# Performance work log

Measured on AMD Instinct MI355X. Metric: run time of the kernel, lower is better.

Reference implementation:

```python
import jax, jax.numpy as jnp
import numpy as np
from jax import lax

K = 10
EPS = 1e-12

def _l2norm(v):
    # F.normalize: v / max(||v||_2, eps) along last dim
    n = jnp.sqrt(jnp.sum(v * v, axis=-1, keepdims=True))
    return v / jnp.maximum(n, EPS)

def setup_inputs() -> dict:
    key = jax.random.key(0)
    ks = jax.random.split(key, 10)
    N, F_in, H, C, E = 100000, 512, 128, 40, 1600000
    x = jax.random.normal(ks[0], (N, F_in), dtype=jnp.float32)
    edge_index = jax.random.randint(ks[1], (2, E), 0, N, dtype=jnp.int64)
    s1 = 1.0 / np.sqrt(F_in)
    W1 = jax.random.uniform(ks[2], (F_in, H), jnp.float32, -s1, s1)
    b1 = jax.random.uniform(ks[3], (H,), jnp.float32, -s1, s1)
    s2 = 1.0 / np.sqrt(H)
    proj_w = jax.random.uniform(ks[4], (H, 1), jnp.float32, -s2, s2)
    proj_b = jax.random.uniform(ks[5], (1,), jnp.float32, -s2, s2)
    hop_w = jax.random.normal(ks[6], (1, K + 1), dtype=jnp.float32) * 0.1  # glorot-ish
    W2 = jax.random.uniform(ks[7], (H, C), jnp.float32, -s2, s2)
    b2 = jax.random.uniform(ks[8], (C,), jnp.float32, -s2, s2)
    return {"x": x, "edge_index": edge_index, "W1": W1, "b1": b1,
            "proj_w": proj_w, "proj_b": proj_b, "hop_w": hop_w,
            "W2": W2, "b2": b2}

def reference(x, edge_index, W1, b1, proj_w, proj_b, hop_w, W2, b2):
    N = x.shape[0]
    # Net: dropout (eval -> identity), lin1 + selu
    h = jax.nn.selu(x @ W1 + b1)  # [N, H]

    # --- gcn_norm with added self-loops ---
    loops = jnp.arange(N, dtype=edge_index.dtype)
    row = jnp.concatenate([edge_index[0], loops])
    col = jnp.concatenate([edge_index[1], loops])
    ew = jnp.ones(row.shape[0], dtype=h.dtype)
    deg = jax.ops.segment_sum(ew, col, num_segments=N)  # [N]
    dinv = jnp.where(deg > 0, lax.rsqrt(deg), 0.0)
    norm = dinv[row] * ew * dinv[col]  # [E+N]

    # --- K hops of scatter-add propagation ---
    def hop(xc, _):
        xn = jax.ops.segment_sum(norm[:, None] * xc[row], col, num_segments=N)
        return xn, xn
    _, hops = lax.scan(hop, h, None, length=K)  # [K, N, H]
    pps = jnp.concatenate([h[None], hops], axis=0).transpose(1, 0, 2)  # [N, K+1, H]

    # attention-weighted hop pooling
    feature_pool = (pps @ proj_w + proj_b)[..., 0]      # [N, K+1]
    m = feature_pool.mean(axis=0)                        # [K+1]
    share_w = _l2norm(m + hop_w)                         # [1, K+1]
    self_w = _l2norm(feature_pool)                       # [N, K+1]
    share = jnp.einsum('k,nkh->nh', share_w[0], pps)     # [N, H]
    selfr = jnp.einsum('nk,nkh->nh', self_w, pps)        # [N, H]
    out_prop = 0.2 * share + 0.8 * selfr

    h2 = jnp.tanh(out_prop)
    logits = h2 @ W2 + b2
    return jax.nn.log_softmax(logits, axis=1)
```

## Files before the change

kernel.cpp:

```cpp
#include <hip/hip_runtime.h>

typedef unsigned int uint;
typedef unsigned short ushort;

typedef short short8 __attribute__((ext_vector_type(8)));
typedef float floatx4 __attribute__((ext_vector_type(4)));

#define FIN 512
#define HF  128
#define NC  40
#define KHOPS 10

__device__ __forceinline__ ushort f2bf(float f) {
    uint u = __float_as_uint(f);
    uint r = (u + 0x7fffu + ((u >> 16) & 1u)) >> 16;
    return (ushort)r;
}
__device__ __forceinline__ float bflo(uint v) { return __uint_as_float(v << 16); }
__device__ __forceinline__ float bfhi(uint v) { return __uint_as_float(v & 0xffff0000u); }
__device__ __forceinline__ uint packbf2(float a, float b) {
    return (uint)f2bf(a) | ((uint)f2bf(b) << 16);
}
__device__ __forceinline__ float selu_f(float v) {
    const float l = 1.0507009873554805f, a = 1.6732632423543772f;
    return v > 0.f ? l * v : l * a * (expf(v) - 1.f);
}

__global__ void k_w1frag(const float* __restrict__ W1, ushort* __restrict__ w1f) {
    int id = blockIdx.x * 256 + threadIdx.x;
    if (id >= 16 * 8 * 64) return;
    int l = id & 63;
    int t = (id >> 6) & 7;
    int s = id >> 9;
    int row0 = s * 32 + (l >> 4) * 8;
    int col  = t * 16 + (l & 15);
    ushort* dst = w1f + (size_t)id * 8;
#pragma unroll
    for (int i = 0; i < 8; ++i)
        dst[i] = f2bf(W1[(row0 + i) * HF + col]);
}

__global__ void k_w2frag(const float* __restrict__ W2, ushort* __restrict__ w2f) {
    int id = blockIdx.x * 256 + threadIdx.x;
    if (id >= 12 * 64) return;
    int l = id & 63;
    int tile = id >> 6;
    int kk = tile / 3, t = tile % 3;
    int row0 = kk * 32 + (l >> 4) * 8;
    int col  = t * 16 + (l & 15);
    ushort* dst = w2f + (size_t)id * 8;
#pragma unroll
    for (int i = 0; i < 8; ++i)
        dst[i] = (col < NC) ? f2bf(W2[(row0 + i) * NC + col]) : (ushort)0;
}

__global__ void k_gemm(const float* __restrict__ x, const ushort* __restrict__ w1f,
                       const float* __restrict__ b1, ushort* __restrict__ h, int N) {
    __shared__ __align__(16) ushort As[64 * 64];
    int tid = threadIdx.x;
    int lane = tid & 63, w = tid >> 6;
    int rowblk = blockIdx.x * 64;

    floatx4 acc[8];
#pragma unroll
    for (int t = 0; t < 8; ++t) acc[t] = (floatx4){0.f, 0.f, 0.f, 0.f};

    for (int kk = 0; kk < 8; ++kk) {
#pragma unroll
        for (int i = 0; i < 4; ++i) {
            int li = tid + 256 * i;
            int r = li >> 4, c4 = li & 15;
            float4 v = make_float4(0.f, 0.f, 0.f, 0.f);
            if (rowblk + r < N)
                v = *(const float4*)(x + (size_t)(rowblk + r) * FIN + kk * 64 + c4 * 4);
            uint p0 = packbf2(v.x, v.y);
            uint p1 = packbf2(v.z, v.w);
            int byteoff = (r * 128 + c4 * 8) ^ ((r & 7) << 4);
            *(uint2*)((char*)As + byteoff) = make_uint2(p0, p1);
        }
        __syncthreads();
        int rowA = w * 16 + (lane & 15);
#pragma unroll
        for (int s = 0; s < 2; ++s) {
            int aoff = (rowA * 128 + s * 64 + (lane >> 4) * 16) ^ ((rowA & 7) << 4);
            short8 af = *(const short8*)((const char*)As + aoff);
#pragma unroll
            for (int t = 0; t < 8; ++t) {
                const short8 bf = *(const short8*)(w1f + ((size_t)((kk * 2 + s) * 8 + t) * 64 + lane) * 8);
                acc[t] = __builtin_amdgcn_mfma_f32_16x16x32_bf16(af, bf, acc[t], 0, 0, 0);
            }
        }
        __syncthreads();
    }
#pragma unroll
    for (int t = 0; t < 8; ++t) {
        int col = t * 16 + (lane & 15);
        float bias = b1[col];
#pragma unroll
        for (int q = 0; q < 4; ++q) {
            int row = rowblk + w * 16 + (lane >> 4) * 4 + q;
            if (row < N) {
                float v = selu_f(acc[t][q] + bias);
                h[(size_t)row * HF + col] = f2bf(v);
            }
        }
    }
}

__global__ void k_deg_init(int* __restrict__ deg, int N) {
    int i = blockIdx.x * 256 + threadIdx.x;
    if (i < N) deg[i] = 1;
}
__global__ void k_deg(const int* __restrict__ ei, int* __restrict__ deg, int E) {
    int e = blockIdx.x * 256 + threadIdx.x;
    if (e < E) atomicAdd(&deg[ei[E + e]], 1);
}
__global__ void k_dinv(const int* __restrict__ deg, float* __restrict__ dinv, int N) {
    int i = blockIdx.x * 256 + threadIdx.x;
    if (i < N) dinv[i] = rsqrtf((float)deg[i]);
}

__global__ void k_scan1(const int* __restrict__ deg, int* __restrict__ offs,
                        int* __restrict__ bsum, int N) {
    __shared__ int lds[256];
    int tid = threadIdx.x;
    int base = blockIdx.x * 1024;
    int c[4], s = 0;
#pragma unroll
    for (int i = 0; i < 4; ++i) {
        int g = base + tid * 4 + i;
        c[i] = (g < N) ? (deg[g] - 1) : 0;
        s += c[i];
    }
    lds[tid] = s;
    __syncthreads();
    for (int off = 1; off < 256; off <<= 1) {
        int add = (tid >= off) ? lds[tid - off] : 0;
        __syncthreads();
        lds[tid] += add;
        __syncthreads();
    }
    int run = lds[tid] - s;
#pragma unroll
    for (int i = 0; i < 4; ++i) {
        int g = base + tid * 4 + i;
        if (g < N) offs[g] = run;
        run += c[i];
    }
    if (tid == 0) bsum[blockIdx.x] = lds[255];
}
__global__ void k_scan2(int* __restrict__ bsum, int nb) {
    if (blockIdx.x == 0 && threadIdx.x == 0) {
        int run = 0;
        for (int i = 0; i < nb; ++i) { int v = bsum[i]; bsum[i] = run; run += v; }
    }
}
__global__ void k_scan3(int* __restrict__ offs, const int* __restrict__ bsum, int N, int E) {
    int g = blockIdx.x * 256 + threadIdx.x;
    if (g < N) offs[g] += bsum[g >> 10];
    else if (g == N) offs[N] = E;
}

__global__ void k_fill(const int* __restrict__ ei, const int* __restrict__ offs,
                       int* __restrict__ cursor, int2* __restrict__ edat,
                       const float* __restrict__ dinv, int E) {
    int e = blockIdx.x * 256 + threadIdx.x;
    if (e >= E) return;
    int r = ei[e], c = ei[E + e];
    int p = offs[c] + atomicAdd(&cursor[c], 1);
    edat[p] = make_int2(r, __float_as_int(dinv[r] * dinv[c]));
}

__global__ void k_fp0(const ushort* __restrict__ h, const float* __restrict__ projw,
                      const float* __restrict__ projb, float* __restrict__ fp0, int N) {
    int wid = (blockIdx.x * blockDim.x + threadIdx.x) >> 6;
    int lane = threadIdx.x & 63;
    if (wid >= N) return;
    uint v = ((const uint*)h)[(size_t)wid * 64 + lane];
    float dot = bflo(v) * projw[2 * lane] + bfhi(v) * projw[2 * lane + 1];
#pragma unroll
    for (int m = 1; m < 64; m <<= 1) dot += __shfl_xor(dot, m);
    if (lane == 0) fp0[wid] = dot + projb[0];
}

__global__ __launch_bounds__(256) void k_hop(
                      const ushort* __restrict__ xin, ushort* __restrict__ xout,
                      const int* __restrict__ offs, const int2* __restrict__ edat,
                      const float* __restrict__ dinv,
                      const float* __restrict__ projw, const float* __restrict__ projb,
                      float* __restrict__ fpk, int N) {
    int wid = (blockIdx.x * blockDim.x + threadIdx.x) >> 6;
    int lane = threadIdx.x & 63;
    if (wid >= N) return;
    const uint* xin2 = (const uint*)xin;
    float dn = dinv[wid];
    uint sv = xin2[(size_t)wid * 64 + lane];
    float wself = dn * dn;
    float acc0 = wself * bflo(sv);
    float acc1 = wself * bfhi(sv);
    int s = offs[wid], e = offs[wid + 1];
    for (int base = s; base < e; base += 64) {
        int idx = base + lane;
        int idxc = min(idx, e - 1);
        int2 ed = edat[idxc];
        int src = ed.x;
        float ew = (idx < e) ? __int_as_float(ed.y) : 0.f;
        int cnt = min(64, e - base);
        int groups = (cnt + 15) >> 4;
        for (int g = 0; g < groups; ++g) {
            int j = g * 16;
            uint xv[16];
            float wv[16];
#pragma unroll
            for (int u = 0; u < 16; ++u) {
                int sj = __builtin_amdgcn_readlane(src, j + u);
                wv[u] = __int_as_float(__builtin_amdgcn_readlane(__float_as_int(ew), j + u));
                xv[u] = xin2[(size_t)(uint)sj * 64 + lane];
            }
#pragma unroll
            for (int u = 0; u < 16; ++u) {
                acc0 = fmaf(wv[u], bflo(xv[u]), acc0);
                acc1 = fmaf(wv[u], bfhi(xv[u]), acc1);
            }
        }
    }
    ((uint*)xout)[(size_t)wid * 64 + lane] = packbf2(acc0, acc1);
    float dot = acc0 * projw[2 * lane] + acc1 * projw[2 * lane + 1];
#pragma unroll
    for (int m = 1; m < 64; m <<= 1) dot += __shfl_xor(dot, m);
    if (lane == 0) fpk[wid] = dot + projb[0];
}

__global__ void k_msum(const float* __restrict__ fp, float* __restrict__ msum, int N) {
    int k = blockIdx.y;
    int i = blockIdx.x * 256 + threadIdx.x;
    int tid = threadIdx.x;
    float v = (i < N) ? fp[(size_t)k * N + i] : 0.f;
#pragma unroll
    for (int m = 1; m < 64; m <<= 1) v += __shfl_xor(v, m);
    __shared__ float ws4[4];
    if ((tid & 63) == 0) ws4[tid >> 6] = v;
    __syncthreads();
    if (tid == 0) atomicAdd(&msum[k], ws4[0] + ws4[1] + ws4[2] + ws4[3]);
}

__global__ void k_sharew(const float* __restrict__ msum, const float* __restrict__ hopw,
                         float* __restrict__ sharew, int N) {
    int k = threadIdx.x;
    float s = (k < KHOPS + 1) ? (msum[k] / (float)N + hopw[k]) : 0.f;
    float ss = s * s;
#pragma unroll
    for (int m = 1; m < 64; m <<= 1) ss += __shfl_xor(ss, m);
    float inv = 1.f / fmaxf(sqrtf(ss), 1e-12f);
    if (k < KHOPS + 1) sharew[k] = s * inv;
}

__global__ __launch_bounds__(256) void k_out(
                     const ushort* __restrict__ hops, const float* __restrict__ fp,
                     const float* __restrict__ sharew, const ushort* __restrict__ w2f,
                     const float* __restrict__ b2, float* __restrict__ out, int N) {
    __shared__ __align__(16) char As[16 * 256];
    int tid = threadIdx.x;
    int nloc = tid >> 4;
    int fg = tid & 15;
    int node = blockIdx.x * 16 + nloc;
    bool valid = node < N;
    int nodec = valid ? node : N - 1;
    const uint* hops2 = (const uint*)hops;

    float c[KHOPS + 1];
    float ss = 0.f;
#pragma unroll
    for (int k = 0; k <= KHOPS; ++k) {
        float f = fp[(size_t)k * N + nodec];
        c[k] = f;
        ss += f * f;
    }
    float inv = 1.f / fmaxf(sqrtf(ss), 1e-12f);
#pragma unroll
    for (int k = 0; k <= KHOPS; ++k)
        c[k] = valid ? (0.2f * sharew[k] + 0.8f * c[k] * inv) : 0.f;

    const uint* base = hops2 + (size_t)nodec * 64 + fg * 4;
    size_t kstr = (size_t)N * 64;
    float a[8];
#pragma unroll
    for (int j = 0; j < 8; ++j) a[j] = 0.f;
#pragma unroll
    for (int k = 0; k <= KHOPS; ++k) {
        uint4 v = *(const uint4*)(base + (size_t)k * kstr);
        float ck = c[k];
        a[0] = fmaf(ck, bflo(v.x), a[0]);
        a[1] = fmaf(ck, bfhi(v.x), a[1]);
        a[2] = fmaf(ck, bflo(v.y), a[2]);
        a[3] = fmaf(ck, bfhi(v.y), a[3]);
        a[4] = fmaf(ck, bflo(v.z), a[4]);
        a[5] = fmaf(ck, bfhi(v.z), a[5]);
        a[6] = fmaf(ck, bflo(v.w), a[6]);
        a[7] = fmaf(ck, bfhi(v.w), a[7]);
    }
    uint4 pk;
    pk.x = packbf2(tanhf(a[0]), tanhf(a[1]));
    pk.y = packbf2(tanhf(a[2]), tanhf(a[3]));
    pk.z = packbf2(tanhf(a[4]), tanhf(a[5]));
    pk.w = packbf2(tanhf(a[6]), tanhf(a[7]));
    {
        int slotbyte = fg * 16;
        int addr = nloc * 256 + (slotbyte ^ ((nloc & 15) << 4));
        *(uint4*)(As + addr) = pk;
    }
    __syncthreads();

    int w = tid >> 6, lane = tid & 63;
    floatx4 acc = (floatx4){0.f, 0.f, 0.f, 0.f};
    if (w < 3) {
        int r = lane & 15;
#pragma unroll
        for (int kk = 0; kk < 4; ++kk) {
            int slotbyte = kk * 64 + (lane >> 4) * 16;
            int addr = r * 256 + (slotbyte ^ ((r & 15) << 4));
            short8 af = *(const short8*)(As + addr);
            const short8 bf = *(const short8*)(w2f + (size_t)((kk * 3 + w) * 64 + lane) * 8);
            acc = __builtin_amdgcn_mfma_f32_16x16x32_bf16(af, bf, acc, 0, 0, 0);
        }
    }
    __syncthreads();

    float* Ls = (float*)As;
    if (w < 3) {
        int cls = w * 16 + (lane & 15);
        float bb = (cls < NC) ? b2[cls] : 0.f;
#pragma unroll
        for (int q = 0; q < 4; ++q) {
            int row = (lane >> 4) * 4 + q;
            Ls[row * 48 + cls] = acc[q] + bb;
        }
    }
    __syncthreads();

    int r2 = tid >> 4;
    int c16 = tid & 15;
    float v0 = Ls[r2 * 48 + c16];
    float v1 = Ls[r2 * 48 + 16 + c16];
    bool has2 = c16 < 8;
    float v2 = has2 ? Ls[r2 * 48 + 32 + c16] : -INFINITY;
    float lm = fmaxf(fmaxf(v0, v1), v2);
#pragma unroll
    for (int m = 1; m < 16; m <<= 1) lm = fmaxf(lm, __shfl_xor(lm, m));
    float se = expf(v0 - lm) + expf(v1 - lm) + (has2 ? expf(v2 - lm) : 0.f);
#pragma unroll
    for (int m = 1; m < 16; m <<= 1) se += __shfl_xor(se, m);
    float lse = lm + logf(se);
    int nodeo = blockIdx.x * 16 + r2;
    if (nodeo < N) {
        out[(size_t)nodeo * NC + c16] = v0 - lse;
        out[(size_t)nodeo * NC + 16 + c16] = v1 - lse;
        if (has2) out[(size_t)nodeo * NC + 32 + c16] = v2 - lse;
    }
}

extern "C" void kernel_launch(void* const* d_in, const int* in_sizes, int n_in,
                              void* d_out, int out_size, void* d_ws, size_t ws_size,
                              hipStream_t stream) {
    const float* x     = (const float*)d_in[0];
    const int*   ei    = (const int*)d_in[1];
    const float* W1    = (const float*)d_in[2];
    const float* b1    = (const float*)d_in[3];
    const float* projw = (const float*)d_in[4];
    const float* projb = (const float*)d_in[5];
    const float* hopw  = (const float*)d_in[6];
    const float* W2    = (const float*)d_in[7];
    const float* b2    = (const float*)d_in[8];
    float* out = (float*)d_out;

    int N = in_sizes[0] / FIN;
    int E = in_sizes[1] / 2;

    char* p = (char*)d_ws;
    auto alloc = [&](size_t bytes) -> char* {
        char* r = p;
        p += (bytes + 255) & ~(size_t)255;
        return r;
    };
    ushort* hops   = (ushort*)alloc((size_t)(KHOPS + 1) * N * HF * 2);
    int*    deg    = (int*)alloc((size_t)N * 4);
    float*  dinv   = (float*)alloc((size_t)N * 4);
    int*    offs   = (int*)alloc((size_t)(N + 1) * 4);
    int*    cursor = (int*)alloc((size_t)N * 4);
    int*    bsum   = (int*)alloc(4096);
    int2*   edat   = (int2*)alloc((size_t)E * 8);
    float*  fp     = (float*)alloc((size_t)(KHOPS + 1) * N * 4);
    float*  msum   = (float*)alloc(64);
    float*  sharew = (float*)alloc(64);
    ushort* w1f    = (ushort*)alloc((size_t)FIN * HF * 2);
    ushort* w2f    = (ushort*)alloc((size_t)12 * 64 * 8 * 2);

    int nb256N = (N + 255) / 256;
    int nbE    = (E + 255) / 256;
    int nbWave = (N + 3) / 4;
    int nb1024 = (N + 1023) / 1024;

    k_w1frag<<<32, 256, 0, stream>>>(W1, w1f);
    k_w2frag<<<3, 256, 0, stream>>>(W2, w2f);
    k_gemm<<<(N + 63) / 64, 256, 0, stream>>>(x, w1f, b1, hops, N);

    k_deg_init<<<nb256N, 256, 0, stream>>>(deg, N);
    k_deg<<<nbE, 256, 0, stream>>>(ei, deg, E);
    k_dinv<<<nb256N, 256, 0, stream>>>(deg, dinv, N);

    k_scan1<<<nb1024, 256, 0, stream>>>(deg, offs, bsum, N);
    k_scan2<<<1, 64, 0, stream>>>(bsum, nb1024);
    k_scan3<<<(N + 256) / 256, 256, 0, stream>>>(offs, bsum, N, E);

    hipMemsetAsync(cursor, 0, (size_t)N * 4, stream);
    k_fill<<<nbE, 256, 0, stream>>>(ei, offs, cursor, edat, dinv, E);

    k_fp0<<<nbWave, 256, 0, stream>>>(hops, projw, projb, fp, N);

    for (int k = 1; k <= KHOPS; ++k) {
        const ushort* xin = hops + (size_t)(k - 1) * N * HF;
        ushort* xout      = hops + (size_t)k * N * HF;
        k_hop<<<nbWave, 256, 0, stream>>>(xin, xout, offs, edat, dinv,
                                          projw, projb, fp + (size_t)k * N, N);
    }

    hipMemsetAsync(msum, 0, 64, stream);
    dim3 gm(nb256N, KHOPS + 1);
    k_msum<<<gm, 256, 0, stream>>>(fp, msum, N);
    k_sharew<<<1, 64, 0, stream>>>(msum, hopw, sharew, N);

    k_out<<<(N + 15) / 16, 256, 0, stream>>>(hops, fp, sharew, w2f, b2, out, N);
}
```

Baseline: 1.009 ms.

## Rewrite lin1 GEMM without LDS, fuse fp0 projection, widen hop gather batches

The lin1 GEMM drops its shared-memory staging. Each wave now loads x rows straight into registers, converts them with v_cvt_pk_bf16_f32, and software-prefetches the next K slice of A and the W1 fragments. Each wave covers 32 rows, so a block covers 128. The hop-0 projection dot product is computed in the GEMM epilogue, which removes the separate k_fp0 kernel and its re-read of h. The hop kernel now handles small neighbor lists with one 16-wide batch and larger ones in 32-wide batches, putting more gathers in flight at the cost of more registers.

```diff
diff --git a/kernel.cpp b/kernel.cpp
--- a/kernel.cpp
+++ b/kernel.cpp
@@ -5,6 +5,7 @@
 
 typedef short short8 __attribute__((ext_vector_type(8)));
 typedef float floatx4 __attribute__((ext_vector_type(4)));
+typedef uint uintx4 __attribute__((ext_vector_type(4)));
 
 #define FIN 512
 #define HF  128
@@ -20,6 +21,11 @@
 __device__ __forceinline__ float bfhi(uint v) { return __uint_as_float(v & 0xffff0000u); }
 __device__ __forceinline__ uint packbf2(float a, float b) {
     return (uint)f2bf(a) | ((uint)f2bf(b) << 16);
+}
+__device__ __forceinline__ uint cvtpk(float lo, float hi) {
+    uint r;
+    asm("v_cvt_pk_bf16_f32 %0, %1, %2" : "=v"(r) : "v"(lo), "v"(hi));
+    return r;
 }
 __device__ __forceinline__ float selu_f(float v) {
     const float l = 1.0507009873554805f, a = 1.6732632423543772f;
@@ -54,56 +60,113 @@
         dst[i] = (col < NC) ? f2bf(W2[(row0 + i) * NC + col]) : (ushort)0;
 }
 
-__global__ void k_gemm(const float* __restrict__ x, const ushort* __restrict__ w1f,
-                       const float* __restrict__ b1, ushort* __restrict__ h, int N) {
-    __shared__ __align__(16) ushort As[64 * 64];
+__global__ __launch_bounds__(256) void k_gemm(
+        const float* __restrict__ x, const ushort* __restrict__ w1f,
+        const float* __restrict__ b1, ushort* __restrict__ h,
+        const float* __restrict__ projw, const float* __restrict__ projb,
+        float* __restrict__ fp0, int N) {
     int tid = threadIdx.x;
     int lane = tid & 63, w = tid >> 6;
-    int rowblk = blockIdx.x * 64;
-
-    floatx4 acc[8];
-#pragma unroll
-    for (int t = 0; t < 8; ++t) acc[t] = (floatx4){0.f, 0.f, 0.f, 0.f};
-
-    for (int kk = 0; kk < 8; ++kk) {
-#pragma unroll
-        for (int i = 0; i < 4; ++i) {
-            int li = tid + 256 * i;
-            int r = li >> 4, c4 = li & 15;
-            float4 v = make_float4(0.f, 0.f, 0.f, 0.f);
-            if (rowblk + r < N)
-                v = *(const float4*)(x + (size_t)(rowblk + r) * FIN + kk * 64 + c4 * 4);
-            uint p0 = packbf2(v.x, v.y);
-            uint p1 = packbf2(v.z, v.w);
-            int byteoff = (r * 128 + c4 * 8) ^ ((r & 7) << 4);
-            *(uint2*)((char*)As + byteoff) = make_uint2(p0, p1);
-        }
-        __syncthreads();
-        int rowA = w * 16 + (lane & 15);
-#pragma unroll
-        for (int s = 0; s < 2; ++s) {
-            int aoff = (rowA * 128 + s * 64 + (lane >> 4) * 16) ^ ((rowA & 7) << 4);
-            short8 af = *(const short8*)((const char*)As + aoff);
-#pragma unroll
-            for (int t = 0; t < 8; ++t) {
-                const short8 bf = *(const short8*)(w1f + ((size_t)((kk * 2 + s) * 8 + t) * 64 + lane) * 8);
-                acc[t] = __builtin_amdgcn_mfma_f32_16x16x32_bf16(af, bf, acc[t], 0, 0, 0);
+    int rowblk = blockIdx.x * 128 + w * 32;
+    int kq = (lane >> 4) * 8;
+
+    int r0 = rowblk + (lane & 15);
+    int r1 = r0 + 16;
+    size_t r0c = (size_t)min(r0, N - 1) * FIN;
+    size_t r1c = (size_t)min(r1, N - 1) * FIN;
+
+    floatx4 acc[2][8];
+#pragma unroll
+    for (int rt = 0; rt < 2; ++rt)
+#pragma unroll
+        for (int t = 0; t < 8; ++t) acc[rt][t] = (floatx4){0.f, 0.f, 0.f, 0.f};
+
+    float4 aC[4];
+    short8 bC[8];
+    {
+        const float* p0 = x + r0c + kq;
+        const float* p1 = x + r1c + kq;
+        aC[0] = *(const float4*)p0; aC[1] = *(const float4*)(p0 + 4);
+        aC[2] = *(const float4*)p1; aC[3] = *(const float4*)(p1 + 4);
+        const ushort* wp = w1f + ((size_t)lane) * 8;
+#pragma unroll
+        for (int t = 0; t < 8; ++t) bC[t] = *(const short8*)(wp + (size_t)t * 512);
+    }
+
+#pragma unroll 1
+    for (int kk = 0; kk < 16; ++kk) {
+        float4 aN[4];
+        short8 bN[8];
+        if (kk < 15) {
+            int kb = (kk + 1) * 32 + kq;
+            const float* p0 = x + r0c + kb;
+            const float* p1 = x + r1c + kb;
+            aN[0] = *(const float4*)p0; aN[1] = *(const float4*)(p0 + 4);
+            aN[2] = *(const float4*)p1; aN[3] = *(const float4*)(p1 + 4);
+            const ushort* wp = w1f + ((size_t)((kk + 1) * 8) * 64 + lane) * 8;
+#pragma unroll
+            for (int t = 0; t < 8; ++t) bN[t] = *(const short8*)(wp + (size_t)t * 512);
+        }
+        uintx4 pa0, pa1;
+        pa0.x = cvtpk(aC[0].x, aC[0].y); pa0.y = cvtpk(aC[0].z, aC[0].w);
+        pa0.z = cvtpk(aC[1].x, aC[1].y); pa0.w = cvtpk(aC[1].z, aC[1].w);
+        pa1.x = cvtpk(aC[2].x, aC[2].y); pa1.y = cvtpk(aC[2].z, aC[2].w);
+        pa1.z = cvtpk(aC[3].x, aC[3].y); pa1.w = cvtpk(aC[3].z, aC[3].w);
+        short8 af0 = __builtin_bit_cast(short8, pa0);
+        short8 af1 = __builtin_bit_cast(short8, pa1);
+#pragma unroll
+        for (int t = 0; t < 8; ++t) {
+            acc[0][t] = __builtin_amdgcn_mfma_f32_16x16x32_bf16(af0, bC[t], acc[0][t], 0, 0, 0);
+            acc[1][t] = __builtin_amdgcn_mfma_f32_16x16x32_bf16(af1, bC[t], acc[1][t], 0, 0, 0);
+        }
+        if (kk < 15) {
+#pragma unroll
+            for (int i = 0; i < 4; ++i) aC[i] = aN[i];
+#pragma unroll
+            for (int t = 0; t < 8; ++t) bC[t] = bN[t];
+        }
+    }
+
+    int col0 = lane & 15;
+    float fpd[2][4];
+#pragma unroll
+    for (int rt = 0; rt < 2; ++rt)
+#pragma unroll
+        for (int q = 0; q < 4; ++q) fpd[rt][q] = 0.f;
+#pragma unroll
+    for (int t = 0; t < 8; ++t) {
+        int col = t * 16 + col0;
+        float bias = b1[col];
+        float pw = projw[col];
+#pragma unroll
+        for (int rt = 0; rt < 2; ++rt) {
+#pragma unroll
+            for (int q = 0; q < 4; ++q) {
+                int row = rowblk + rt * 16 + (lane >> 4) * 4 + q;
+                float v = selu_f(acc[rt][t][q] + bias);
+                if (row < N) h[(size_t)row * HF + col] = f2bf(v);
+                fpd[rt][q] = fmaf(v, pw, fpd[rt][q]);
             }
         }
-        __syncthreads();
-    }
-#pragma unroll
-    for (int t = 0; t < 8; ++t) {
-        int col = t * 16 + (lane & 15);
-        float bias = b1[col];
+    }
+#pragma unroll
+    for (int rt = 0; rt < 2; ++rt)
 #pragma unroll
         for (int q = 0; q < 4; ++q) {
-            int row = rowblk + w * 16 + (lane >> 4) * 4 + q;
-            if (row < N) {
-                float v = selu_f(acc[t][q] + bias);
-                h[(size_t)row * HF + col] = f2bf(v);
+            float d = fpd[rt][q];
+#pragma unroll
+            for (int m = 1; m < 16; m <<= 1) d += __shfl_xor(d, m);
+            fpd[rt][q] = d;
+        }
+    if (col0 == 0) {
+        float pb = projb[0];
+#pragma unroll
+        for (int rt = 0; rt < 2; ++rt)
+#pragma unroll
+            for (int q = 0; q < 4; ++q) {
+                int row = rowblk + rt * 16 + (lane >> 4) * 4 + q;
+                if (row < N) fp0[row] = fpd[rt][q] + pb;
             }
-        }
     }
 }
 
@@ -169,18 +232,6 @@
     int r = ei[e], c = ei[E + e];
     int p = offs[c] + atomicAdd(&cursor[c], 1);
     edat[p] = make_int2(r, __float_as_int(dinv[r] * dinv[c]));
-}
-
-__global__ void k_fp0(const ushort* __restrict__ h, const float* __restrict__ projw,
-                      const float* __restrict__ projb, float* __restrict__ fp0, int N) {
-    int wid = (blockIdx.x * blockDim.x + threadIdx.x) >> 6;
-    int lane = threadIdx.x & 63;
-    if (wid >= N) return;
-    uint v = ((const uint*)h)[(size_t)wid * 64 + lane];
-    float dot = bflo(v) * projw[2 * lane] + bfhi(v) * projw[2 * lane + 1];
-#pragma unroll
-    for (int m = 1; m < 64; m <<= 1) dot += __shfl_xor(dot, m);
-    if (lane == 0) fp0[wid] = dot + projb[0];
 }
 
 __global__ __launch_bounds__(256) void k_hop(
@@ -206,21 +257,37 @@
         int src = ed.x;
         float ew = (idx < e) ? __int_as_float(ed.y) : 0.f;
         int cnt = min(64, e - base);
-        int groups = (cnt + 15) >> 4;
-        for (int g = 0; g < groups; ++g) {
-            int j = g * 16;
+        if (cnt <= 16) {
             uint xv[16];
             float wv[16];
 #pragma unroll
             for (int u = 0; u < 16; ++u) {
-                int sj = __builtin_amdgcn_readlane(src, j + u);
-                wv[u] = __int_as_float(__builtin_amdgcn_readlane(__float_as_int(ew), j + u));
+                int sj = __builtin_amdgcn_readlane(src, u);
+                wv[u] = __int_as_float(__builtin_amdgcn_readlane(__float_as_int(ew), u));
                 xv[u] = xin2[(size_t)(uint)sj * 64 + lane];
             }
 #pragma unroll
             for (int u = 0; u < 16; ++u) {
                 acc0 = fmaf(wv[u], bflo(xv[u]), acc0);
                 acc1 = fmaf(wv[u], bfhi(xv[u]), acc1);
+            }
+        } else {
+            int groups = (cnt + 31) >> 5;
+            for (int g = 0; g < groups; ++g) {
+                int j = g * 32;
+                uint xv[32];
+                float wv[32];
+#pragma unroll
+                for (int u = 0; u < 32; ++u) {
+                    int sj = __builtin_amdgcn_readlane(src, j + u);
+                    wv[u] = __int_as_float(__builtin_amdgcn_readlane(__float_as_int(ew), j + u));
+                    xv[u] = xin2[(size_t)(uint)sj * 64 + lane];
+                }
+#pragma unroll
+                for (int u = 0; u < 32; ++u) {
+                    acc0 = fmaf(wv[u], bflo(xv[u]), acc0);
+                    acc1 = fmaf(wv[u], bfhi(xv[u]), acc1);
+                }
             }
         }
     }
@@ -402,7 +469,7 @@
 
     k_w1frag<<<32, 256, 0, stream>>>(W1, w1f);
     k_w2frag<<<3, 256, 0, stream>>>(W2, w2f);
-    k_gemm<<<(N + 63) / 64, 256, 0, stream>>>(x, w1f, b1, hops, N);
+    k_gemm<<<(N + 127) / 128, 256, 0, stream>>>(x, w1f, b1, hops, projw, projb, fp, N);
 
     k_deg_init<<<nb256N, 256, 0, stream>>>(deg, N);
     k_deg<<<nbE, 256, 0, stream>>>(ei, deg, E);
@@ -414,8 +481,6 @@
 
     hipMemsetAsync(cursor, 0, (size_t)N * 4, stream);
     k_fill<<<nbE, 256, 0, stream>>>(ei, offs, cursor, edat, dinv, E);
-
-    k_fp0<<<nbWave, 256, 0, stream>>>(hops, projw, projb, fp, N);
 
     for (int k = 1; k <= KHOPS; ++k) {
         const ushort* xin = hops + (size_t)(k - 1) * N * HF;
```

After: 1.029 ms. +2.0%, slower.
